# Performance work log

Measured on AMD Instinct MI355X. Metric: run time of the kernel, lower is better.

Reference implementation:

```python
import jax, jax.numpy as jnp
import numpy as np

N_NODES = 100000
N_EDGES = 1600000
D_IN = 128
D_HID = 128
N_CLASSES = 64


def _sage_mean_layer(h, src, dst, deg, W_self, W_neigh, b):
    # gather source-node features along edges: [E, d]
    msg = h[src]
    # sum messages into destination nodes, then mean by in-degree
    agg = jax.ops.segment_sum(msg, dst, num_segments=N_NODES)
    mean_neigh = agg / deg[:, None]
    return jax.nn.relu(h @ W_self + mean_neigh @ W_neigh + b)


def setup_inputs() -> dict:
    key = jax.random.key(0)
    ks = jax.random.split(key, 9)
    s = 1.0 / np.sqrt(D_IN)
    return {
        "features": jax.random.normal(ks[0], (N_NODES, D_IN), dtype=jnp.float32),
        "src": jax.random.randint(ks[1], (N_EDGES,), 0, N_NODES, dtype=jnp.int32),
        "dst": jax.random.randint(ks[2], (N_EDGES,), 0, N_NODES, dtype=jnp.int32),
        "W_self1": jax.random.normal(ks[3], (D_IN, D_HID), dtype=jnp.float32) * s,
        "W_neigh1": jax.random.normal(ks[4], (D_IN, D_HID), dtype=jnp.float32) * s,
        "b1": jnp.zeros((D_HID,), dtype=jnp.float32),
        "W_self2": jax.random.normal(ks[5], (D_HID, D_HID), dtype=jnp.float32) * s,
        "W_neigh2": jax.random.normal(ks[6], (D_HID, D_HID), dtype=jnp.float32) * s,
        "b2": jnp.zeros((D_HID,), dtype=jnp.float32),
        "W_out": jax.random.normal(ks[7], (D_HID, N_CLASSES), dtype=jnp.float32) * s,
        "b_out": jnp.zeros((N_CLASSES,), dtype=jnp.float32),
    }


def reference(features, src, dst, W_self1, W_neigh1, b1, W_self2, W_neigh2, b2, W_out, b_out):
    # in-degree per destination node (clamped to avoid div-by-zero for isolated nodes)
    deg = jax.ops.segment_sum(jnp.ones((N_EDGES,), jnp.float32), dst, num_segments=N_NODES)
    deg = jnp.maximum(deg, 1.0)
    h = _sage_mean_layer(features, src, dst, deg, W_self1, W_neigh1, b1)
    h = _sage_mean_layer(h, src, dst, deg, W_self2, W_neigh2, b2)
    return h @ W_out + b_out  # [N_NODES, N_CLASSES] logits
```

## Files before the change

kernel.cpp:

```cpp
#include <hip/hip_runtime.h>
#include <hip/hip_bf16.h>

constexpr int N_NODES = 100000;
constexpr int N_EDGES = 1600000;
constexpr int D = 128;
constexpr int N_CLASSES = 64;

constexpr int PART_NODES = 32;
constexpr int NPART = N_NODES / PART_NODES;
constexpr int NB1 = 49;
constexpr int CAP1 = 40960;
constexpr int SUBB = 10;
constexpr int CHUNK = CAP1 / SUBB;
constexpr int CAP2 = 1024;
constexpr int NCTR2 = NB1 * 64;
constexpr int EB1 = (N_EDGES + 1023) / 1024;
constexpr int CVTB = N_NODES * (D / 4) / 256;
constexpr int PKB = 36;

typedef __attribute__((ext_vector_type(8))) short short8;
typedef __attribute__((ext_vector_type(4))) float f32x4;
typedef __attribute__((ext_vector_type(2))) float f32x2;

static __device__ __forceinline__ float bf2f(unsigned int lo16) {
    unsigned int x = lo16 << 16;
    return __builtin_bit_cast(float, x);
}
static __device__ __forceinline__ unsigned short f2bf(float f) {
    unsigned int x = __builtin_bit_cast(unsigned int, f);
    x += 0x7fffu + ((x >> 16) & 1u);
    return (unsigned short)(x >> 16);
}
static __device__ __forceinline__ unsigned int pack4_fp8(float a, float b,
                                                         float c, float d) {
    int v = __builtin_amdgcn_cvt_pk_fp8_f32(a, b, 0, false);
    v = __builtin_amdgcn_cvt_pk_fp8_f32(c, d, v, true);
    return (unsigned int)v;
}
static __device__ __forceinline__ unsigned char f2fp8(float a) {
    return (unsigned char)(__builtin_amdgcn_cvt_pk_fp8_f32(a, a, 0, false) & 0xff);
}
static __device__ __forceinline__ void dec8(uint2 u, float* acc) {
    f32x2 q;
    q = __builtin_amdgcn_cvt_pk_f32_fp8(u.x, false); acc[0] += q[0]; acc[1] += q[1];
    q = __builtin_amdgcn_cvt_pk_f32_fp8(u.x, true);  acc[2] += q[0]; acc[3] += q[1];
    q = __builtin_amdgcn_cvt_pk_f32_fp8(u.y, false); acc[4] += q[0]; acc[5] += q[1];
    q = __builtin_amdgcn_cvt_pk_f32_fp8(u.y, true);  acc[6] += q[0]; acc[7] += q[1];
}

__global__ __launch_bounds__(256) void prep_k(const int* __restrict__ src,
                                              const int* __restrict__ dst,
                                              int* __restrict__ cursor1,
                                              unsigned int* __restrict__ pack1,
                                              const float* __restrict__ feat,
                                              unsigned short* __restrict__ fbuf,
                                              unsigned int* __restrict__ f8buf,
                                              const float* __restrict__ Ws1,
                                              const float* __restrict__ Wn1,
                                              const float* __restrict__ Ws2,
                                              const float* __restrict__ Wn2,
                                              const float* __restrict__ Wo,
                                              unsigned short* __restrict__ wp1,
                                              unsigned short* __restrict__ wp2,
                                              unsigned short* __restrict__ wpo) {
    __shared__ unsigned int lpay[1024];
    __shared__ unsigned char lcb[1024];
    __shared__ int hist[NB1], loff[NB1], gpos[NB1], lcur[NB1];

    const int b = blockIdx.x;
    const int t = threadIdx.x;

    if (b < EB1) {
        const int ebase = b * 1024;
        int nblk = N_EDGES - ebase;
        if (nblk > 1024) nblk = 1024;
        const bool ok = (t * 4 < nblk);

        if (t < NB1) hist[t] = 0;
        __syncthreads();

        int4 d4, s4;
        if (ok) {
            d4 = *(const int4*)(dst + ebase + t * 4);
            s4 = *(const int4*)(src + ebase + t * 4);
            atomicAdd(&hist[d4.x >> 11], 1);
            atomicAdd(&hist[d4.y >> 11], 1);
            atomicAdd(&hist[d4.z >> 11], 1);
            atomicAdd(&hist[d4.w >> 11], 1);
        }
        __syncthreads();

        if (t == 0) {
            int run = 0;
            #pragma unroll
            for (int k = 0; k < NB1; ++k) { loff[k] = run; run += hist[k]; }
        }
        __syncthreads();
        if (t < NB1) {
            gpos[t] = atomicAdd(cursor1 + t, hist[t]);
            lcur[t] = loff[t];
        }
        __syncthreads();

        if (ok) {
            #pragma unroll
            for (int k = 0; k < 4; ++k) {
                int dd = (k == 0) ? d4.x : (k == 1) ? d4.y : (k == 2) ? d4.z : d4.w;
                int ss = (k == 0) ? s4.x : (k == 1) ? s4.y : (k == 2) ? s4.z : s4.w;
                int cb = dd >> 11;
                int pos = atomicAdd(&lcur[cb], 1);
                lpay[pos] = ((unsigned int)(dd & 2047) << 17) | (unsigned int)ss;
                lcb[pos] = (unsigned char)cb;
            }
        }
        __syncthreads();

        for (int i = t; i < nblk; i += 256) {
            int cb = lcb[i];
            int rel = gpos[cb] + (i - loff[cb]);
            if (rel < CAP1) pack1[(size_t)cb * CAP1 + rel] = lpay[i];
        }
    } else if (b < EB1 + CVTB) {
        int i = (b - EB1) * 256 + t;
        float4 v = ((const float4*)feat)[i];
        ushort4 r;
        r.x = f2bf(v.x); r.y = f2bf(v.y); r.z = f2bf(v.z); r.w = f2bf(v.w);
        ((ushort4*)fbuf)[i] = r;
        f8buf[i] = pack4_fp8(v.x, v.y, v.z, v.w);
    } else {
        int g = (b - EB1 - CVTB) * 4 + (t >> 6);
        if (g >= 144) return;
        int lane = t & 63;
        const float *Wa, *Wb;
        unsigned short* wp;
        int DOUT, bb;
        if (g < 64)       { Wa = Ws1; Wb = Wn1; wp = wp1; DOUT = 128; bb = g; }
        else if (g < 128) { Wa = Ws2; Wb = Wn2; wp = wp2; DOUT = 128; bb = g - 64; }
        else              { Wa = Wo;  Wb = nullptr; wp = wpo; DOUT = 64; bb = g - 128; }
        int NCT = DOUT / 16;
        int kstep = bb / NCT;
        int ct = bb % NCT;
        int col = ct * 16 + (lane & 15);
        int kbase = kstep * 32 + (lane >> 4) * 8;
        unsigned short r[8];
        #pragma unroll
        for (int j = 0; j < 8; ++j) {
            int k = kbase + j;
            float w = (k < 128) ? Wa[(size_t)k * DOUT + col]
                                : Wb[(size_t)(k - 128) * DOUT + col];
            r[j] = f2bf(w);
        }
        *(short8*)(wp + ((size_t)((kstep * NCT + ct) * 64 + lane)) * 8) =
            *(const short8*)r;
    }
}

__global__ __launch_bounds__(256) void bin2_k(const int* __restrict__ cursor1,
                                              int* __restrict__ cursor2,
                                              const unsigned int* __restrict__ pack1,
                                              unsigned int* __restrict__ pack2) {
    __shared__ unsigned int lpay[CHUNK];
    __shared__ unsigned int lsort[CHUNK];
    __shared__ int hist[64], loff[64], gpos[64], lcur[64];

    const int t = threadIdx.x;
    const int cb = blockIdx.x / SUBB;
    const int sb = blockIdx.x % SUBB;

    int cnt = cursor1[cb];
    if (cnt > CAP1) cnt = CAP1;
    const int base = sb * CHUNK;
    int n = cnt - base;
    if (n <= 0) return;
    if (n > CHUNK) n = CHUNK;

    if (t < 64) hist[t] = 0;
    __syncthreads();

    const unsigned int* gsrc = pack1 + (size_t)cb * CAP1 + base;
    for (int i = t; i < n; i += 256) {
        unsigned int pk = gsrc[i];
        lpay[i] = pk;
        atomicAdd(&hist[pk >> 22], 1);
    }
    __syncthreads();

    if (t == 0) {
        int run = 0;
        #pragma unroll
        for (int k = 0; k < 64; ++k) { loff[k] = run; run += hist[k]; }
    }
    __syncthreads();
    if (t < 64) {
        gpos[t] = atomicAdd(cursor2 + cb * 64 + t, hist[t]);
        lcur[t] = loff[t];
    }
    __syncthreads();

    for (int i = t; i < n; i += 256) {
        unsigned int pk = lpay[i];
        int pos = atomicAdd(&lcur[pk >> 22], 1);
        lsort[pos] = pk;
    }
    __syncthreads();

    for (int i = t; i < n; i += 256) {
        unsigned int pk = lsort[i];
        int pw = pk >> 22;
        int p = cb * 64 + pw;
        int rel = gpos[pw] + (i - loff[pw]);
        if (rel < CAP2) pack2[((size_t)p << 10) + rel] = pk & 0x003fffffu;
    }
}

template <bool OUTPROJ>
__global__ __launch_bounds__(256) void fused_k(const unsigned short* __restrict__ xin,
                                               const unsigned char* __restrict__ x8,
                                               const unsigned int* __restrict__ pack,
                                               const int* __restrict__ cursor2,
                                               const short8* __restrict__ wp,
                                               const float* __restrict__ bias,
                                               unsigned short* __restrict__ xout,
                                               unsigned char* __restrict__ x8out,
                                               const short8* __restrict__ wpo,
                                               const float* __restrict__ bout,
                                               float* __restrict__ outp) {
    __shared__ unsigned int eraw[CAP2];
    __shared__ unsigned int ssrc[CAP2];
    __shared__ int nsh;
    __shared__ int bcnt[32];
    __shared__ int boff[33];
    __shared__ unsigned short mlds[PART_NODES][136];

    const int t = threadIdx.x;
    const int p = blockIdx.x;

    if (t == 0) {
        int c = cursor2[p];
        nsh = (c < CAP2) ? c : CAP2;
    }
    if (t < 32) bcnt[t] = 0;
    __syncthreads();
    const int n = nsh;

    const unsigned int* gsrc = pack + ((size_t)p << 10);
    for (int i = t; i < n; i += 256) {
        unsigned int pk = gsrc[i];
        eraw[i] = pk;
        atomicAdd(&bcnt[pk >> 17], 1);
    }
    __syncthreads();

    if (t == 0) {
        int s = 0;
        #pragma unroll
        for (int i = 0; i < 32; ++i) { boff[i] = s; s += bcnt[i]; }
        boff[32] = s;
    }
    __syncthreads();
    if (t < 32) bcnt[t] = boff[t];
    __syncthreads();

    for (int i = t; i < n; i += 256) {
        unsigned int pk = eraw[i];
        int pos = atomicAdd(&bcnt[pk >> 17], 1);
        ssrc[pos] = pk & 0x1ffffu;
    }
    __syncthreads();

    const int w = t >> 6, lane = t & 63;
    const int sub = lane >> 4;
    const int cl8 = (lane & 15) * 8;
    const int cl = lane & 15;

    for (int g = 0; g < 8; ++g) {
        const int ni = w * 8 + g;
        const int b = boff[ni];
        const int eN = boff[ni + 1];

        float acc[8];
        #pragma unroll
        for (int r = 0; r < 8; ++r) acc[r] = 0.f;

        int i = b + sub;
        for (; i + 12 < eN; i += 16) {
            unsigned s0 = ssrc[i], s1 = ssrc[i + 4], s2 = ssrc[i + 8], s3 = ssrc[i + 12];
            uint2 u0 = *(const uint2*)(x8 + ((s0 << 7) + cl8));
            uint2 u1 = *(const uint2*)(x8 + ((s1 << 7) + cl8));
            uint2 u2 = *(const uint2*)(x8 + ((s2 << 7) + cl8));
            uint2 u3 = *(const uint2*)(x8 + ((s3 << 7) + cl8));
            dec8(u0, acc); dec8(u1, acc); dec8(u2, acc); dec8(u3, acc);
        }
        for (; i + 4 < eN; i += 8) {
            unsigned s0 = ssrc[i], s1 = ssrc[i + 4];
            uint2 u0 = *(const uint2*)(x8 + ((s0 << 7) + cl8));
            uint2 u1 = *(const uint2*)(x8 + ((s1 << 7) + cl8));
            dec8(u0, acc); dec8(u1, acc);
        }
        if (i < eN) {
            unsigned s0 = ssrc[i];
            uint2 u0 = *(const uint2*)(x8 + ((s0 << 7) + cl8));
            dec8(u0, acc);
        }
        #pragma unroll
        for (int r = 0; r < 8; ++r) {
            acc[r] += __shfl_xor(acc[r], 16);
            acc[r] += __shfl_xor(acc[r], 32);
        }
        float inv = 1.0f / fmaxf((float)(eN - b), 1.0f);
        float lo = acc[sub * 2 + 0] * inv;
        float hi = acc[sub * 2 + 1] * inv;
        unsigned int o = ((unsigned int)f2bf(hi) << 16) | (unsigned int)f2bf(lo);
        *(unsigned int*)(&mlds[ni][cl * 8 + sub * 2]) = o;
    }
    __syncthreads();

    const int frag = w & 1;
    const int cg0 = (w >> 1) * 4;
    const int r15 = lane & 15;
    const int khi = lane >> 4;
    const int row0 = p * PART_NODES + frag * 16;
    const unsigned short* arow = xin + (size_t)(row0 + r15) * 128 + khi * 8;

    f32x4 acc[4];
    #pragma unroll
    for (int c = 0; c < 4; ++c) acc[c] = {0.f, 0.f, 0.f, 0.f};

    #pragma unroll
    for (int ks = 0; ks < 8; ++ks) {
        short8 a;
        if (ks < 4) a = *(const short8*)(arow + ks * 32);
        else        a = *(const short8*)(&mlds[frag * 16 + r15][(ks - 4) * 32 + khi * 8]);
        #pragma unroll
        for (int c = 0; c < 4; ++c) {
            short8 b = wp[(ks * 8 + cg0 + c) * 64 + lane];
            acc[c] = __builtin_amdgcn_mfma_f32_16x16x32_bf16(a, b, acc[c], 0, 0, 0);
        }
    }

    const int rhi = khi, col0 = r15;
    if (!OUTPROJ) {
        #pragma unroll
        for (int c = 0; c < 4; ++c) {
            float bv = bias[(cg0 + c) * 16 + col0];
            #pragma unroll
            for (int j = 0; j < 4; ++j) {
                float v = fmaxf(acc[c][j] + bv, 0.f);
                size_t off = (size_t)(row0 + rhi * 4 + j) * 128 + (cg0 + c) * 16 + col0;
                xout[off] = f2bf(v);
                x8out[off] = f2fp8(v);
            }
        }
    } else {
        __syncthreads();
        #pragma unroll
        for (int c = 0; c < 4; ++c) {
            float bv = bias[(cg0 + c) * 16 + col0];
            #pragma unroll
            for (int j = 0; j < 4; ++j) {
                float v = fmaxf(acc[c][j] + bv, 0.f);
                mlds[frag * 16 + rhi * 4 + j][(cg0 + c) * 16 + col0] = f2bf(v);
            }
        }
        __syncthreads();
        const int frag2 = w & 1;
        const int ct0 = (w >> 1) * 2;
        f32x4 oacc[2];
        oacc[0] = {0.f, 0.f, 0.f, 0.f};
        oacc[1] = {0.f, 0.f, 0.f, 0.f};
        #pragma unroll
        for (int ks = 0; ks < 4; ++ks) {
            short8 a = *(const short8*)(&mlds[frag2 * 16 + r15][ks * 32 + khi * 8]);
            #pragma unroll
            for (int c = 0; c < 2; ++c) {
                short8 b = wpo[(ks * 4 + ct0 + c) * 64 + lane];
                oacc[c] = __builtin_amdgcn_mfma_f32_16x16x32_bf16(a, b, oacc[c], 0, 0, 0);
            }
        }
        #pragma unroll
        for (int c = 0; c < 2; ++c) {
            float bv = bout[(ct0 + c) * 16 + col0];
            #pragma unroll
            for (int j = 0; j < 4; ++j) {
                outp[(size_t)(p * PART_NODES + frag2 * 16 + rhi * 4 + j) * N_CLASSES
                     + (ct0 + c) * 16 + col0] = oacc[c][j] + bv;
            }
        }
    }
}

extern "C" void kernel_launch(void* const* d_in, const int* in_sizes, int n_in,
                              void* d_out, int out_size, void* d_ws, size_t ws_size,
                              hipStream_t stream) {
    const float* feat   = (const float*)d_in[0];
    const int*   src    = (const int*)d_in[1];
    const int*   dst    = (const int*)d_in[2];
    const float* Wself1 = (const float*)d_in[3];
    const float* Wneigh1= (const float*)d_in[4];
    const float* b1     = (const float*)d_in[5];
    const float* Wself2 = (const float*)d_in[6];
    const float* Wneigh2= (const float*)d_in[7];
    const float* b2     = (const float*)d_in[8];
    const float* Wout   = (const float*)d_in[9];
    const float* bout   = (const float*)d_in[10];
    float* out = (float*)d_out;
    (void)ws_size;

    int* cursor1 = (int*)d_ws;
    int* cursor2 = cursor1 + 64;
    unsigned int* pack1 = (unsigned int*)(cursor2 + NCTR2);
    unsigned int* pack2 = pack1 + (size_t)NB1 * CAP1;
    unsigned short* fbuf1 = (unsigned short*)(pack2 + (size_t)NCTR2 * CAP2);
    unsigned short* h1    = fbuf1 + (size_t)N_NODES * D;
    unsigned int* f8feat  = (unsigned int*)(h1 + (size_t)N_NODES * D);
    unsigned int* h1f8    = f8feat + (size_t)N_NODES * (D / 4);
    unsigned short* wp1   = (unsigned short*)(h1f8 + (size_t)N_NODES * (D / 4));
    unsigned short* wp2   = wp1 + 256 * 128;
    unsigned short* wpo   = wp2 + 256 * 128;

    hipMemsetAsync(cursor1, 0, (64 + NCTR2) * sizeof(int), stream);

    prep_k<<<EB1 + CVTB + PKB, 256, 0, stream>>>(src, dst, cursor1, pack1,
                                                 feat, fbuf1, f8feat,
                                                 Wself1, Wneigh1, Wself2, Wneigh2,
                                                 Wout, wp1, wp2, wpo);

    bin2_k<<<NB1 * SUBB, 256, 0, stream>>>(cursor1, cursor2, pack1, pack2);

    fused_k<false><<<NPART, 256, 0, stream>>>(fbuf1, (const unsigned char*)f8feat,
                                              pack2, cursor2,
                                              (const short8*)wp1, b1, h1,
                                              (unsigned char*)h1f8,
                                              nullptr, nullptr, nullptr);

    fused_k<true><<<NPART, 256, 0, stream>>>(h1, (const unsigned char*)h1f8,
                                             pack2, cursor2,
                                             (const short8*)wp2, b2, nullptr, nullptr,
                                             (const short8*)wpo, bout, out);
}
```

Measured before the change: 190.7 us.

## Double edge-bucketing block size and drop 4-way gather unroll

The edge bucketing phase in prep_k now processes 2048 edges per block (8 per thread, two int4 loads each of src and dst) instead of 1024, which halves the number of blocks and the global cursor atomics. Separately, the neighbour gather loop in the aggregation kernel drops its 16-stride four-load unroll, keeps only the two-load loop, and switches to size_t address arithmetic. Fewer loads in flight per thread can reduce memory-level parallelism in the gather. The larger edge blocks double shared staging per block and lower parallelism in the prep phase.

```diff
diff --git a/kernel.cpp b/kernel.cpp
--- a/kernel.cpp
+++ b/kernel.cpp
@@ -14,7 +14,8 @@
 constexpr int CHUNK = CAP1 / SUBB;
 constexpr int CAP2 = 1024;
 constexpr int NCTR2 = NB1 * 64;
-constexpr int EB1 = (N_EDGES + 1023) / 1024;
+constexpr int BE = 2048;
+constexpr int EB1 = (N_EDGES + BE - 1) / BE;
 constexpr int CVTB = N_NODES * (D / 4) / 256;
 constexpr int PKB = 36;
 
@@ -63,30 +64,36 @@
                                               unsigned short* __restrict__ wp1,
                                               unsigned short* __restrict__ wp2,
                                               unsigned short* __restrict__ wpo) {
-    __shared__ unsigned int lpay[1024];
-    __shared__ unsigned char lcb[1024];
+    __shared__ unsigned int lpay[BE];
+    __shared__ unsigned char lcb[BE];
     __shared__ int hist[NB1], loff[NB1], gpos[NB1], lcur[NB1];
 
     const int b = blockIdx.x;
     const int t = threadIdx.x;
 
     if (b < EB1) {
-        const int ebase = b * 1024;
+        const int ebase = b * BE;
         int nblk = N_EDGES - ebase;
-        if (nblk > 1024) nblk = 1024;
-        const bool ok = (t * 4 < nblk);
+        if (nblk > BE) nblk = BE;
+        const bool ok = (t * 8 < nblk);
 
         if (t < NB1) hist[t] = 0;
         __syncthreads();
 
-        int4 d4, s4;
+        int4 d4a, s4a, d4b, s4b;
         if (ok) {
-            d4 = *(const int4*)(dst + ebase + t * 4);
-            s4 = *(const int4*)(src + ebase + t * 4);
-            atomicAdd(&hist[d4.x >> 11], 1);
-            atomicAdd(&hist[d4.y >> 11], 1);
-            atomicAdd(&hist[d4.z >> 11], 1);
-            atomicAdd(&hist[d4.w >> 11], 1);
+            d4a = *(const int4*)(dst + ebase + t * 8);
+            d4b = *(const int4*)(dst + ebase + t * 8 + 4);
+            s4a = *(const int4*)(src + ebase + t * 8);
+            s4b = *(const int4*)(src + ebase + t * 8 + 4);
+            atomicAdd(&hist[d4a.x >> 11], 1);
+            atomicAdd(&hist[d4a.y >> 11], 1);
+            atomicAdd(&hist[d4a.z >> 11], 1);
+            atomicAdd(&hist[d4a.w >> 11], 1);
+            atomicAdd(&hist[d4b.x >> 11], 1);
+            atomicAdd(&hist[d4b.y >> 11], 1);
+            atomicAdd(&hist[d4b.z >> 11], 1);
+            atomicAdd(&hist[d4b.w >> 11], 1);
         }
         __syncthreads();
 
@@ -104,9 +111,15 @@
 
         if (ok) {
             #pragma unroll
-            for (int k = 0; k < 4; ++k) {
-                int dd = (k == 0) ? d4.x : (k == 1) ? d4.y : (k == 2) ? d4.z : d4.w;
-                int ss = (k == 0) ? s4.x : (k == 1) ? s4.y : (k == 2) ? s4.z : s4.w;
+            for (int k = 0; k < 8; ++k) {
+                int dd, ss;
+                if (k < 4) {
+                    dd = (k == 0) ? d4a.x : (k == 1) ? d4a.y : (k == 2) ? d4a.z : d4a.w;
+                    ss = (k == 0) ? s4a.x : (k == 1) ? s4a.y : (k == 2) ? s4a.z : s4a.w;
+                } else {
+                    dd = (k == 4) ? d4b.x : (k == 5) ? d4b.y : (k == 6) ? d4b.z : d4b.w;
+                    ss = (k == 4) ? s4b.x : (k == 5) ? s4b.y : (k == 6) ? s4b.z : s4b.w;
+                }
                 int cb = dd >> 11;
                 int pos = atomicAdd(&lcur[cb], 1);
                 lpay[pos] = ((unsigned int)(dd & 2047) << 17) | (unsigned int)ss;
@@ -270,7 +283,6 @@
 
     const int w = t >> 6, lane = t & 63;
     const int sub = lane >> 4;
-    const int cl8 = (lane & 15) * 8;
     const int cl = lane & 15;
 
     for (int g = 0; g < 8; ++g) {
@@ -283,23 +295,17 @@
         for (int r = 0; r < 8; ++r) acc[r] = 0.f;
 
         int i = b + sub;
-        for (; i + 12 < eN; i += 16) {
-            unsigned s0 = ssrc[i], s1 = ssrc[i + 4], s2 = ssrc[i + 8], s3 = ssrc[i + 12];
-            uint2 u0 = *(const uint2*)(x8 + ((s0 << 7) + cl8));
-            uint2 u1 = *(const uint2*)(x8 + ((s1 << 7) + cl8));
-            uint2 u2 = *(const uint2*)(x8 + ((s2 << 7) + cl8));
-            uint2 u3 = *(const uint2*)(x8 + ((s3 << 7) + cl8));
-            dec8(u0, acc); dec8(u1, acc); dec8(u2, acc); dec8(u3, acc);
-        }
         for (; i + 4 < eN; i += 8) {
-            unsigned s0 = ssrc[i], s1 = ssrc[i + 4];
-            uint2 u0 = *(const uint2*)(x8 + ((s0 << 7) + cl8));
-            uint2 u1 = *(const uint2*)(x8 + ((s1 << 7) + cl8));
-            dec8(u0, acc); dec8(u1, acc);
+            int s0 = ssrc[i];
+            int s1 = ssrc[i + 4];
+            uint2 u0 = *(const uint2*)(x8 + (size_t)s0 * 128 + cl * 8);
+            uint2 u1 = *(const uint2*)(x8 + (size_t)s1 * 128 + cl * 8);
+            dec8(u0, acc);
+            dec8(u1, acc);
         }
         if (i < eN) {
-            unsigned s0 = ssrc[i];
-            uint2 u0 = *(const uint2*)(x8 + ((s0 << 7) + cl8));
+            int s0 = ssrc[i];
+            uint2 u0 = *(const uint2*)(x8 + (size_t)s0 * 128 + cl * 8);
             dec8(u0, acc);
         }
         #pragma unroll
```

Result: faster. 164.3 us (-13.8%).
